# Kernel tuning notes

Measured on AMD Instinct MI355X. Metric: run time of the kernel, lower is better.

Reference implementation:

```python
import jax, jax.numpy as jnp
import numpy as np
import math

NUM_HEADS = 4
NUM_GROUPS = 16
EPS = 1e-5


def setup_inputs() -> dict:
    key = jax.random.key(0)
    ks = jax.random.split(key, 4)
    C = 256
    x = jax.random.normal(ks[0], (1, C, 16, 16, 16), dtype=jnp.float32)
    gn_gamma = jnp.ones((C,), dtype=jnp.float32)
    gn_beta = jnp.zeros((C,), dtype=jnp.float32)
    # conv3d 1x1 kernels == plain matrices [out_ch, in_ch]
    w_qkv = jax.random.normal(ks[1], (3 * C, C), dtype=jnp.float32) * (1.0 / math.sqrt(C))
    w_proj = jax.random.normal(ks[2], (C, C), dtype=jnp.float32) * (1.0 / math.sqrt(C))
    b_proj = jnp.zeros((C,), dtype=jnp.float32)
    return {"x": x, "gn_gamma": gn_gamma, "gn_beta": gn_beta,
            "w_qkv": w_qkv, "w_proj": w_proj, "b_proj": b_proj}


def reference(x, gn_gamma, gn_beta, w_qkv, w_proj, b_proj):
    B, C, H, W, D = x.shape
    N = H * W * D
    heads = NUM_HEADS
    d = C // heads

    xf = x.reshape(B, C, N)  # [B, C, N]

    # GroupNorm(16, C) with affine params
    xg = xf.reshape(B, NUM_GROUPS, C // NUM_GROUPS, N)
    mu = jnp.mean(xg, axis=(2, 3), keepdims=True)
    var = jnp.var(xg, axis=(2, 3), keepdims=True)
    xn = ((xg - mu) * jax.lax.rsqrt(var + EPS)).reshape(B, C, N)
    xn = xn * gn_gamma[None, :, None] + gn_beta[None, :, None]

    # 1x1 conv QKV: [B, 3C, N]
    qkv = jnp.einsum('oc,bcn->bon', w_qkv, xn)
    # torch: qkv.reshape(B*heads, 3d, N).chunk(3, dim=1)
    qkv = qkv.reshape(B * heads, 3 * d, N)
    q, k, v = qkv[:, :d], qkv[:, d:2 * d], qkv[:, 2 * d:]

    scale = 1.0 / math.sqrt(math.sqrt(d))
    attn = jnp.einsum('bct,bcs->bts', q * scale, k * scale)  # [B*heads, N, N]
    attn = jax.nn.softmax(attn, axis=-1)
    h = jnp.einsum('bts,bcs->bct', attn, v)  # [B*heads, d, N]

    h = h.reshape(B, C, N)
    out = jnp.einsum('oc,bcn->bon', w_proj, h) + b_proj[None, :, None]
    return (out + xf).reshape(B, C, H, W, D)
```

## Files before the change

### kernel.cpp

```cpp
#include <hip/hip_runtime.h>
#include <math.h>

#define N_TOK 4096
#define C_CH  256
#define SPLITS 4

typedef short bf16x8 __attribute__((ext_vector_type(8)));
typedef float f32x4  __attribute__((ext_vector_type(4)));
typedef unsigned short u16;

__device__ __forceinline__ u16 f2bf(float f) {
    union { float f; unsigned u; } v; v.f = f;
    unsigned r = v.u + 0x7FFF + ((v.u >> 16) & 1);
    return (u16)(r >> 16);
}
__device__ __forceinline__ float bf2f(u16 b) {
    union { unsigned u; float f; } v; v.u = ((unsigned)b) << 16;
    return v.f;
}
__device__ __forceinline__ unsigned packtr(float a, float b) {
    union { float f; unsigned u; } ua, ub; ua.f = a; ub.f = b;
    return __builtin_amdgcn_perm(ub.u, ua.u, 0x07060302u);
}

__global__ __launch_bounds__(256) void wcvt(const float* __restrict__ wqkv,
                                            const float* __restrict__ wproj,
                                            u16* __restrict__ wq, u16* __restrict__ wp) {
    int i = blockIdx.x * 256 + threadIdx.x;
    if (i < 196608) {
        int row = i >> 8;
        float s = ((row % 192) < 64) ? 0.125f : 1.0f;
        wq[i] = f2bf(wqkv[i] * s);
    } else {
        wp[i - 196608] = f2bf(wproj[i - 196608]);
    }
}

__global__ __launch_bounds__(256) void gn_part(const float* __restrict__ x,
                                               float2* __restrict__ part) {
    const int b = blockIdx.x, tid = threadIdx.x;
    const int lane = tid & 63, wave = tid >> 6;
    const float4* xp = (const float4*)x + b * 1024;
    float s = 0.f, ss = 0.f;
#pragma unroll
    for (int k = 0; k < 4; ++k) {
        float4 v = xp[tid + k * 256];
        s  += v.x + v.y + v.z + v.w;
        ss += v.x * v.x + v.y * v.y + v.z * v.z + v.w * v.w;
    }
#pragma unroll
    for (int off = 1; off < 64; off <<= 1) {
        s  += __shfl_xor(s, off, 64);
        ss += __shfl_xor(ss, off, 64);
    }
    __shared__ float rs[4], rss[4];
    if (lane == 0) { rs[wave] = s; rss[wave] = ss; }
    __syncthreads();
    if (tid == 0) part[b] = make_float2(rs[0]+rs[1]+rs[2]+rs[3], rss[0]+rss[1]+rss[2]+rss[3]);
}

__global__ void gn_fin(const float2* __restrict__ part, float* __restrict__ stats) {
    int g = threadIdx.x;
    if (g < 16) {
        float s = 0.f, ss = 0.f;
        for (int j = 0; j < 16; ++j) { float2 p = part[g * 16 + j]; s += p.x; ss += p.y; }
        float mu = s / 65536.f;
        float var = ss / 65536.f - mu * mu;
        stats[g * 2] = mu;
        stats[g * 2 + 1] = rsqrtf(var + 1e-5f);
    }
}

__global__ __launch_bounds__(256) void norm_t(const float* __restrict__ x,
                                              const float* __restrict__ stats,
                                              const float* __restrict__ gamma,
                                              const float* __restrict__ beta,
                                              u16* __restrict__ xt) {
    const int tb = blockIdx.x * 64, cb = blockIdx.y * 64;
    const int tid = threadIdx.x;
    __shared__ float T[64][65];
#pragma unroll
    for (int it = 0; it < 16; ++it) {
        int idx = tid + it * 256;
        int c = idx >> 6, t = idx & 63;
        int cg = cb + c;
        float mu = stats[(cg >> 4) * 2], rstd = stats[(cg >> 4) * 2 + 1];
        T[c][t] = (x[cg * N_TOK + tb + t] - mu) * rstd * gamma[cg] + beta[cg];
    }
    __syncthreads();
#pragma unroll
    for (int it = 0; it < 16; ++it) {
        int idx = tid + it * 256;
        int t = idx >> 6, c = idx & 63;
        xt[(tb + t) * C_CH + cb + c] = f2bf(T[c][t]);
    }
}

__global__ __launch_bounds__(256) void qkv_gemm(const u16* __restrict__ wq,
                                                const u16* __restrict__ xt,
                                                u16* __restrict__ QT,
                                                u16* __restrict__ KTm,
                                                u16* __restrict__ Vc) {
    const int nb = blockIdx.x * 64;
    const int mo = blockIdx.y * 64 + (threadIdx.x >> 6) * 16;
    const int lane = threadIdx.x & 63;
    const int quad = lane >> 4, low = lane & 15;

    f32x4 acc[4] = {f32x4{0,0,0,0}, f32x4{0,0,0,0}, f32x4{0,0,0,0}, f32x4{0,0,0,0}};
#pragma unroll
    for (int kc = 0; kc < 8; ++kc) {
        bf16x8 af = *(const bf16x8*)(wq + (mo + low) * 256 + kc * 32 + quad * 8);
#pragma unroll
        for (int nt = 0; nt < 4; ++nt) {
            bf16x8 bf_ = *(const bf16x8*)(xt + (nb + nt * 16 + low) * 256 + kc * 32 + quad * 8);
            acc[nt] = __builtin_amdgcn_mfma_f32_16x16x32_bf16(af, bf_, acc[nt], 0, 0, 0);
        }
    }
#pragma unroll
    for (int r = 0; r < 4; ++r) {
        int o = mo + quad * 4 + r;
        int head = o / 192, rem = o % 192, c = rem & 63;
#pragma unroll
        for (int nt = 0; nt < 4; ++nt) {
            int tok = nb + nt * 16 + low;
            u16 v = f2bf(acc[nt][r]);
            if (rem < 64)       QT [(head * N_TOK + tok) * 64 + c] = v;
            else if (rem < 128) KTm[(head * N_TOK + tok) * 64 + c] = v;
            else                Vc [(head * 64 + c) * N_TOK + tok] = v;
        }
    }
}

__global__ __launch_bounds__(256, 2) void attn_kernel(const u16* __restrict__ QT,
                                                      const u16* __restrict__ KTm,
                                                      const u16* __restrict__ Vc,
                                                      u16* __restrict__ Op,
                                                      float* __restrict__ Lp) {
    const int head = blockIdx.y, split = blockIdx.z;
    const int qb   = blockIdx.x * 128;
    const int tid  = threadIdx.x;
    const int wave = tid >> 6, lane = tid & 63;
    const int quad = lane >> 4, low = lane & 15;

    const u16* Qh = QT  + head * N_TOK * 64;
    const u16* Kh = KTm + head * N_TOK * 64 + split * 1024 * 64;
    const u16* Vh = Vc  + head * 64 * N_TOK + split * 1024;

    __shared__ u16 Ks[64 * 64];
    __shared__ u16 Vs[64 * 64];
    __shared__ u16 Ps[4 * 32 * 64];
    u16* Pw = Ps + wave * 2048;

    bf16x8 ones;
#pragma unroll
    for (int i = 0; i < 8; ++i) ones[i] = (short)0x3F80;

    bf16x8 bq[2][2];
#pragma unroll
    for (int tn = 0; tn < 2; ++tn)
#pragma unroll
        for (int kh = 0; kh < 2; ++kh)
            bq[tn][kh] = *(const bf16x8*)(Qh + (qb + wave * 32 + tn * 16 + low) * 64 + kh * 32 + quad * 8);

    f32x4 oa[2][4], lC[2];
#pragma unroll
    for (int mt = 0; mt < 2; ++mt) {
        lC[mt] = f32x4{0,0,0,0};
#pragma unroll
        for (int cn = 0; cn < 4; ++cn) oa[mt][cn] = f32x4{0,0,0,0};
    }

    const int sA = tid >> 3, gA = tid & 7;
    const int swA = ((gA ^ (sA & 7)) * 8);
    const int swB = ((gA ^ ((sA + 32) & 7)) * 8);
    uint4 pk0 = *(const uint4*)(Kh + sA * 64 + gA * 8);
    uint4 pk1 = *(const uint4*)(Kh + (sA + 32) * 64 + gA * 8);
    uint4 pv0 = *(const uint4*)(Vh + sA * N_TOK + gA * 8);
    uint4 pv1 = *(const uint4*)(Vh + (sA + 32) * N_TOK + gA * 8);

    const int low7 = low & 7;

    for (int kt = 0; kt < 16; ++kt) {
        __syncthreads();
        *(uint4*)(Ks + sA * 64 + swA) = pk0;
        *(uint4*)(Ks + (sA + 32) * 64 + swB) = pk1;
        *(uint4*)(Vs + sA * 64 + swA) = pv0;
        *(uint4*)(Vs + (sA + 32) * 64 + swB) = pv1;
        if (kt < 15) {
            int sb2 = (kt + 1) * 64;
            pk0 = *(const uint4*)(Kh + (sb2 + sA) * 64 + gA * 8);
            pk1 = *(const uint4*)(Kh + (sb2 + sA + 32) * 64 + gA * 8);
            pv0 = *(const uint4*)(Vh + sA * N_TOK + sb2 + gA * 8);
            pv1 = *(const uint4*)(Vh + (sA + 32) * N_TOK + sb2 + gA * 8);
        }
        __syncthreads();

        f32x4 sa[4][2];
#pragma unroll
        for (int sm = 0; sm < 4; ++sm)
#pragma unroll
            for (int tn = 0; tn < 2; ++tn) sa[sm][tn] = f32x4{0,0,0,0};
#pragma unroll
        for (int kh = 0; kh < 2; ++kh)
#pragma unroll
            for (int sm = 0; sm < 4; ++sm) {
                bf16x8 ak = *(const bf16x8*)(Ks + (sm * 16 + low) * 64 + (((quad + 4 * kh) ^ low7) * 8));
#pragma unroll
                for (int tn = 0; tn < 2; ++tn)
                    sa[sm][tn] = __builtin_amdgcn_mfma_f32_16x16x32_bf16(ak, bq[tn][kh], sa[sm][tn], 0, 0, 0);
            }

#pragma unroll
        for (int sm = 0; sm < 4; ++sm)
#pragma unroll
            for (int tn = 0; tn < 2; ++tn) {
                float p0 = __expf(sa[sm][tn][0]);
                float p1 = __expf(sa[sm][tn][1]);
                float p2 = __expf(sa[sm][tn][2]);
                float p3 = __expf(sa[sm][tn][3]);
                uint2 pk; pk.x = packtr(p0, p1); pk.y = packtr(p2, p3);
                int t = tn * 16 + low;
                int sw = ((sm * 2 + (quad >> 1)) ^ low7);
                *(uint2*)(Pw + t * 64 + sw * 8 + (quad & 1) * 4) = pk;
            }
        asm volatile("s_waitcnt lgkmcnt(0)" ::: "memory");

#pragma unroll
        for (int kh = 0; kh < 2; ++kh) {
            bf16x8 ap0 = *(const bf16x8*)(Pw + (low) * 64      + (((quad + 4 * kh) ^ low7) * 8));
            bf16x8 ap1 = *(const bf16x8*)(Pw + (16 + low) * 64 + (((quad + 4 * kh) ^ low7) * 8));
            lC[0] = __builtin_amdgcn_mfma_f32_16x16x32_bf16(ap0, ones, lC[0], 0, 0, 0);
            lC[1] = __builtin_amdgcn_mfma_f32_16x16x32_bf16(ap1, ones, lC[1], 0, 0, 0);
#pragma unroll
            for (int cn = 0; cn < 4; ++cn) {
                bf16x8 bv = *(const bf16x8*)(Vs + (cn * 16 + low) * 64 + (((quad + 4 * kh) ^ low7) * 8));
                oa[0][cn] = __builtin_amdgcn_mfma_f32_16x16x32_bf16(ap0, bv, oa[0][cn], 0, 0, 0);
                oa[1][cn] = __builtin_amdgcn_mfma_f32_16x16x32_bf16(ap1, bv, oa[1][cn], 0, 0, 0);
            }
        }
    }

    const int sh = (split * 4 + head) * N_TOK;
#pragma unroll
    for (int mt = 0; mt < 2; ++mt)
#pragma unroll
        for (int r = 0; r < 4; ++r) {
            int t = qb + wave * 32 + mt * 16 + quad * 4 + r;
            if (low == 0) Lp[sh + t] = lC[mt][r];
#pragma unroll
            for (int cn = 0; cn < 4; ++cn)
                Op[(sh + t) * 64 + cn * 16 + low] = f2bf(oa[mt][cn][r]);
        }
}

__global__ __launch_bounds__(256) void combine(const u16* __restrict__ Op,
                                               const float* __restrict__ Lp,
                                               u16* __restrict__ hT) {
    int row = blockIdx.x * 4 + (threadIdx.x >> 6);
    int head = row >> 12, t = row & 4095, c = threadIdx.x & 63;
    float o = 0.f, l = 0.f;
#pragma unroll
    for (int sp = 0; sp < SPLITS; ++sp) {
        int b = (sp * 4 + head) * N_TOK + t;
        o += bf2f(Op[b * 64 + c]);
        l += Lp[b];
    }
    hT[t * C_CH + head * 64 + c] = f2bf(o / l);
}

__global__ __launch_bounds__(256) void proj_gemm(const u16* __restrict__ wp,
                                                 const u16* __restrict__ hT,
                                                 const float* __restrict__ bias,
                                                 const float* __restrict__ xres,
                                                 float* __restrict__ out) {
    const int nb = blockIdx.x * 32;
    const int mo = blockIdx.y * 64 + (threadIdx.x >> 6) * 16;
    const int lane = threadIdx.x & 63;
    const int quad = lane >> 4, low = lane & 15;

    f32x4 acc[2] = {f32x4{0,0,0,0}, f32x4{0,0,0,0}};
#pragma unroll
    for (int kc = 0; kc < 8; ++kc) {
        bf16x8 af = *(const bf16x8*)(wp + (mo + low) * 256 + kc * 32 + quad * 8);
#pragma unroll
        for (int nt = 0; nt < 2; ++nt) {
            bf16x8 bf_ = *(const bf16x8*)(hT + (nb + nt * 16 + low) * 256 + kc * 32 + quad * 8);
            acc[nt] = __builtin_amdgcn_mfma_f32_16x16x32_bf16(af, bf_, acc[nt], 0, 0, 0);
        }
    }
#pragma unroll
    for (int r = 0; r < 4; ++r) {
        int o = mo + quad * 4 + r;
        float bv = bias[o];
#pragma unroll
        for (int nt = 0; nt < 2; ++nt) {
            int tok = nb + nt * 16 + low;
            out[o * N_TOK + tok] = acc[nt][r] + bv + xres[o * N_TOK + tok];
        }
    }
}

extern "C" void kernel_launch(void* const* d_in, const int* in_sizes, int n_in,
                              void* d_out, int out_size, void* d_ws, size_t ws_size,
                              hipStream_t stream) {
    const float* x      = (const float*)d_in[0];
    const float* gamma  = (const float*)d_in[1];
    const float* beta   = (const float*)d_in[2];
    const float* w_qkv  = (const float*)d_in[3];
    const float* w_proj = (const float*)d_in[4];
    const float* b_proj = (const float*)d_in[5];
    float* out = (float*)d_out;

    char* base = (char*)d_ws;
    u16*    Op    = (u16*)base;
    u16*    xt    = (u16*)base;
    float*  Lp    = (float*)(base + 8388608);
    float*  stats = (float*)(base + 8650752);
    float2* part  = (float2*)(base + 8654848);
    u16*    wq    = (u16*)(base + 8658944);
    u16*    wp    = (u16*)(base + 9052160);
    u16*    QT    = (u16*)(base + 9183232);
    u16*    hT    = QT;
    u16*    KTm   = (u16*)(base + 11280384);
    u16*    Vc    = (u16*)(base + 13377536);

    wcvt      <<<1024, 256, 0, stream>>>(w_qkv, w_proj, wq, wp);
    gn_part   <<<256, 256, 0, stream>>>(x, part);
    gn_fin    <<<1, 64, 0, stream>>>(part, stats);
    norm_t    <<<dim3(64, 4),  256, 0, stream>>>(x, stats, gamma, beta, xt);
    qkv_gemm  <<<dim3(64, 12), 256, 0, stream>>>(wq, xt, QT, KTm, Vc);
    attn_kernel<<<dim3(32, 4, SPLITS), 256, 0, stream>>>(QT, KTm, Vc, Op, Lp);
    combine   <<<4096, 256, 0, stream>>>(Op, Lp, hT);
    proj_gemm <<<dim3(128, 4), 256, 0, stream>>>(wp, hT, b_proj, x, out);
}
```

Measured before the change: 130.2 us.

## Fuse prep kernels, restructure attention with in-block KV split and register fragments

Merges weight conversion and GroupNorm partial sums into one launch, and folds the group-stat finalization into norm_t. The attention kernel now gives each block 64 queries, with each wave covering an interleaved quarter of the keys. K and V fragments are loaded straight from global memory into double-buffered registers instead of being staged through shared memory. The separate split-combine kernel is replaced by an in-block reduction through shared memory, and exp is swapped for exp2 with the log2e factor folded into the Q weight scale. This drops kernel launches and the Op/Lp round trip, at the cost of fewer attention blocks (256), higher register pressure at occupancy 1, and uncoalesced direct global fragment loads.

```diff
diff --git a/kernel.cpp b/kernel.cpp
--- a/kernel.cpp
+++ b/kernel.cpp
@@ -3,7 +3,6 @@
 
 #define N_TOK 4096
 #define C_CH  256
-#define SPLITS 4
 
 typedef short bf16x8 __attribute__((ext_vector_type(8)));
 typedef float f32x4  __attribute__((ext_vector_type(4)));
@@ -14,78 +13,79 @@
     unsigned r = v.u + 0x7FFF + ((v.u >> 16) & 1);
     return (u16)(r >> 16);
 }
-__device__ __forceinline__ float bf2f(u16 b) {
-    union { unsigned u; float f; } v; v.u = ((unsigned)b) << 16;
-    return v.f;
-}
 __device__ __forceinline__ unsigned packtr(float a, float b) {
     union { float f; unsigned u; } ua, ub; ua.f = a; ub.f = b;
     return __builtin_amdgcn_perm(ub.u, ua.u, 0x07060302u);
 }
 
-__global__ __launch_bounds__(256) void wcvt(const float* __restrict__ wqkv,
+__global__ __launch_bounds__(256) void prep(const float* __restrict__ wqkv,
                                             const float* __restrict__ wproj,
-                                            u16* __restrict__ wq, u16* __restrict__ wp) {
-    int i = blockIdx.x * 256 + threadIdx.x;
-    if (i < 196608) {
-        int row = i >> 8;
-        float s = ((row % 192) < 64) ? 0.125f : 1.0f;
-        wq[i] = f2bf(wqkv[i] * s);
+                                            const float* __restrict__ x,
+                                            u16* __restrict__ wq, u16* __restrict__ wp,
+                                            float2* __restrict__ part) {
+    const int b = blockIdx.x, tid = threadIdx.x;
+    __shared__ float rs[4], rss[4];
+    if (b < 1024) {
+        int i = b * 256 + tid;
+        if (i < 196608) {
+            int row = i >> 8;
+            float s = ((row % 192) < 64) ? 0.18033688f : 1.0f;
+            wq[i] = f2bf(wqkv[i] * s);
+        } else {
+            wp[i - 196608] = f2bf(wproj[i - 196608]);
+        }
     } else {
-        wp[i - 196608] = f2bf(wproj[i - 196608]);
-    }
-}
-
-__global__ __launch_bounds__(256) void gn_part(const float* __restrict__ x,
-                                               float2* __restrict__ part) {
-    const int b = blockIdx.x, tid = threadIdx.x;
-    const int lane = tid & 63, wave = tid >> 6;
-    const float4* xp = (const float4*)x + b * 1024;
-    float s = 0.f, ss = 0.f;
-#pragma unroll
-    for (int k = 0; k < 4; ++k) {
-        float4 v = xp[tid + k * 256];
-        s  += v.x + v.y + v.z + v.w;
-        ss += v.x * v.x + v.y * v.y + v.z * v.z + v.w * v.w;
-    }
-#pragma unroll
-    for (int off = 1; off < 64; off <<= 1) {
-        s  += __shfl_xor(s, off, 64);
-        ss += __shfl_xor(ss, off, 64);
-    }
-    __shared__ float rs[4], rss[4];
-    if (lane == 0) { rs[wave] = s; rss[wave] = ss; }
-    __syncthreads();
-    if (tid == 0) part[b] = make_float2(rs[0]+rs[1]+rs[2]+rs[3], rss[0]+rss[1]+rss[2]+rss[3]);
-}
-
-__global__ void gn_fin(const float2* __restrict__ part, float* __restrict__ stats) {
-    int g = threadIdx.x;
-    if (g < 16) {
+        const int bb = b - 1024;
+        const int lane = tid & 63, wave = tid >> 6;
+        const float4* xp = (const float4*)x + bb * 1024;
         float s = 0.f, ss = 0.f;
-        for (int j = 0; j < 16; ++j) { float2 p = part[g * 16 + j]; s += p.x; ss += p.y; }
-        float mu = s / 65536.f;
-        float var = ss / 65536.f - mu * mu;
-        stats[g * 2] = mu;
-        stats[g * 2 + 1] = rsqrtf(var + 1e-5f);
+#pragma unroll
+        for (int k = 0; k < 4; ++k) {
+            float4 v = xp[tid + k * 256];
+            s  += v.x + v.y + v.z + v.w;
+            ss += v.x * v.x + v.y * v.y + v.z * v.z + v.w * v.w;
+        }
+#pragma unroll
+        for (int off = 1; off < 64; off <<= 1) {
+            s  += __shfl_xor(s, off, 64);
+            ss += __shfl_xor(ss, off, 64);
+        }
+        if (lane == 0) { rs[wave] = s; rss[wave] = ss; }
+        __syncthreads();
+        if (tid == 0) part[bb] = make_float2(rs[0]+rs[1]+rs[2]+rs[3], rss[0]+rss[1]+rss[2]+rss[3]);
     }
 }
 
 __global__ __launch_bounds__(256) void norm_t(const float* __restrict__ x,
-                                              const float* __restrict__ stats,
+                                              const float2* __restrict__ part,
                                               const float* __restrict__ gamma,
                                               const float* __restrict__ beta,
                                               u16* __restrict__ xt) {
     const int tb = blockIdx.x * 64, cb = blockIdx.y * 64;
     const int tid = threadIdx.x;
+    __shared__ float sst[8];
     __shared__ float T[64][65];
+    if (tid < 64) {
+        float2 p = part[(blockIdx.y * 4 + (tid >> 4)) * 16 + (tid & 15)];
+        float s = p.x, ss = p.y;
+#pragma unroll
+        for (int off = 1; off < 16; off <<= 1) {
+            s += __shfl_xor(s, off, 64); ss += __shfl_xor(ss, off, 64);
+        }
+        if ((tid & 15) == 0) {
+            float mu = s / 65536.f;
+            float var = ss / 65536.f - mu * mu;
+            sst[(tid >> 4) * 2] = mu;
+            sst[(tid >> 4) * 2 + 1] = rsqrtf(var + 1e-5f);
+        }
+    }
+    __syncthreads();
 #pragma unroll
     for (int it = 0; it < 16; ++it) {
         int idx = tid + it * 256;
         int c = idx >> 6, t = idx & 63;
-        int cg = cb + c;
-        float mu = stats[(cg >> 4) * 2], rstd = stats[(cg >> 4) * 2 + 1];
-        T[c][t] = (x[cg * N_TOK + tb + t] - mu) * rstd * gamma[cg] + beta[cg];
+        int cg = cb + c, gl = c >> 4;
+        T[c][t] = (x[cg * N_TOK + tb + t] - sst[gl * 2]) * sst[gl * 2 + 1] * gamma[cg] + beta[cg];
     }
     __syncthreads();
 #pragma unroll
@@ -131,141 +131,150 @@
     }
 }
 
-__global__ __launch_bounds__(256, 2) void attn_kernel(const u16* __restrict__ QT,
+struct Frags { bf16x8 ak[4][2]; bf16x8 bv[2][4]; };
+
+__global__ __launch_bounds__(256, 1) void attn_kernel(const u16* __restrict__ QT,
                                                       const u16* __restrict__ KTm,
                                                       const u16* __restrict__ Vc,
-                                                      u16* __restrict__ Op,
-                                                      float* __restrict__ Lp) {
-    const int head = blockIdx.y, split = blockIdx.z;
-    const int qb   = blockIdx.x * 128;
+                                                      u16* __restrict__ hT) {
+    const int head = blockIdx.y;
+    const int qb   = blockIdx.x * 64;
     const int tid  = threadIdx.x;
     const int wave = tid >> 6, lane = tid & 63;
     const int quad = lane >> 4, low = lane & 15;
+    const int low7 = low & 7;
 
     const u16* Qh = QT  + head * N_TOK * 64;
-    const u16* Kh = KTm + head * N_TOK * 64 + split * 1024 * 64;
-    const u16* Vh = Vc  + head * 64 * N_TOK + split * 1024;
-
-    __shared__ u16 Ks[64 * 64];
-    __shared__ u16 Vs[64 * 64];
-    __shared__ u16 Ps[4 * 32 * 64];
-    u16* Pw = Ps + wave * 2048;
+    const u16* Kh = KTm + head * N_TOK * 64;
+    const u16* Vh = Vc  + head * 64 * N_TOK;
+
+    __shared__ union {
+        u16 ps[4][4096];
+        struct { float buf[2][64][65]; float lb[2][64]; } cb;
+    } sm;
+    u16* Pw = sm.ps[wave];
 
     bf16x8 ones;
 #pragma unroll
     for (int i = 0; i < 8; ++i) ones[i] = (short)0x3F80;
 
-    bf16x8 bq[2][2];
-#pragma unroll
-    for (int tn = 0; tn < 2; ++tn)
+    bf16x8 bq[4][2];
+#pragma unroll
+    for (int tn = 0; tn < 4; ++tn)
 #pragma unroll
         for (int kh = 0; kh < 2; ++kh)
-            bq[tn][kh] = *(const bf16x8*)(Qh + (qb + wave * 32 + tn * 16 + low) * 64 + kh * 32 + quad * 8);
-
-    f32x4 oa[2][4], lC[2];
-#pragma unroll
-    for (int mt = 0; mt < 2; ++mt) {
-        lC[mt] = f32x4{0,0,0,0};
-#pragma unroll
-        for (int cn = 0; cn < 4; ++cn) oa[mt][cn] = f32x4{0,0,0,0};
-    }
-
-    const int sA = tid >> 3, gA = tid & 7;
-    const int swA = ((gA ^ (sA & 7)) * 8);
-    const int swB = ((gA ^ ((sA + 32) & 7)) * 8);
-    uint4 pk0 = *(const uint4*)(Kh + sA * 64 + gA * 8);
-    uint4 pk1 = *(const uint4*)(Kh + (sA + 32) * 64 + gA * 8);
-    uint4 pv0 = *(const uint4*)(Vh + sA * N_TOK + gA * 8);
-    uint4 pv1 = *(const uint4*)(Vh + (sA + 32) * N_TOK + gA * 8);
-
-    const int low7 = low & 7;
-
-    for (int kt = 0; kt < 16; ++kt) {
-        __syncthreads();
-        *(uint4*)(Ks + sA * 64 + swA) = pk0;
-        *(uint4*)(Ks + (sA + 32) * 64 + swB) = pk1;
-        *(uint4*)(Vs + sA * 64 + swA) = pv0;
-        *(uint4*)(Vs + (sA + 32) * 64 + swB) = pv1;
-        if (kt < 15) {
-            int sb2 = (kt + 1) * 64;
-            pk0 = *(const uint4*)(Kh + (sb2 + sA) * 64 + gA * 8);
-            pk1 = *(const uint4*)(Kh + (sb2 + sA + 32) * 64 + gA * 8);
-            pv0 = *(const uint4*)(Vh + sA * N_TOK + sb2 + gA * 8);
-            pv1 = *(const uint4*)(Vh + (sA + 32) * N_TOK + sb2 + gA * 8);
-        }
-        __syncthreads();
-
-        f32x4 sa[4][2];
-#pragma unroll
-        for (int sm = 0; sm < 4; ++sm)
-#pragma unroll
-            for (int tn = 0; tn < 2; ++tn) sa[sm][tn] = f32x4{0,0,0,0};
+            bq[tn][kh] = *(const bf16x8*)(Qh + (qb + tn * 16 + low) * 64 + kh * 32 + quad * 8);
+
+    f32x4 oa[4][4], lC[4];
+#pragma unroll
+    for (int tm = 0; tm < 4; ++tm) {
+        lC[tm] = f32x4{0,0,0,0};
+#pragma unroll
+        for (int cn = 0; cn < 4; ++cn) oa[tm][cn] = f32x4{0,0,0,0};
+    }
+
+    auto load_frags = [&](Frags& F, int sbase) {
+#pragma unroll
+        for (int sq = 0; sq < 4; ++sq)
+#pragma unroll
+            for (int kh = 0; kh < 2; ++kh)
+                F.ak[sq][kh] = *(const bf16x8*)(Kh + (sbase + sq * 16 + low) * 64 + kh * 32 + quad * 8);
+#pragma unroll
+        for (int f = 0; f < 2; ++f)
+#pragma unroll
+            for (int cn = 0; cn < 4; ++cn)
+                F.bv[f][cn] = *(const bf16x8*)(Vh + (cn * 16 + low) * N_TOK + sbase + f * 32 + quad * 8);
+    };
+
+    auto compute_tile = [&](const Frags& F) {
+        f32x4 sa[4][4];
+#pragma unroll
+        for (int sq = 0; sq < 4; ++sq)
+#pragma unroll
+            for (int tn = 0; tn < 4; ++tn) sa[sq][tn] = f32x4{0,0,0,0};
 #pragma unroll
         for (int kh = 0; kh < 2; ++kh)
 #pragma unroll
-            for (int sm = 0; sm < 4; ++sm) {
-                bf16x8 ak = *(const bf16x8*)(Ks + (sm * 16 + low) * 64 + (((quad + 4 * kh) ^ low7) * 8));
-#pragma unroll
-                for (int tn = 0; tn < 2; ++tn)
-                    sa[sm][tn] = __builtin_amdgcn_mfma_f32_16x16x32_bf16(ak, bq[tn][kh], sa[sm][tn], 0, 0, 0);
-            }
-
-#pragma unroll
-        for (int sm = 0; sm < 4; ++sm)
-#pragma unroll
-            for (int tn = 0; tn < 2; ++tn) {
-                float p0 = __expf(sa[sm][tn][0]);
-                float p1 = __expf(sa[sm][tn][1]);
-                float p2 = __expf(sa[sm][tn][2]);
-                float p3 = __expf(sa[sm][tn][3]);
+            for (int sq = 0; sq < 4; ++sq)
+#pragma unroll
+                for (int tn = 0; tn < 4; ++tn)
+                    sa[sq][tn] = __builtin_amdgcn_mfma_f32_16x16x32_bf16(F.ak[sq][kh], bq[tn][kh], sa[sq][tn], 0, 0, 0);
+#pragma unroll
+        for (int sq = 0; sq < 4; ++sq)
+#pragma unroll
+            for (int tn = 0; tn < 4; ++tn) {
+                float p0 = __builtin_amdgcn_exp2f(sa[sq][tn][0]);
+                float p1 = __builtin_amdgcn_exp2f(sa[sq][tn][1]);
+                float p2 = __builtin_amdgcn_exp2f(sa[sq][tn][2]);
+                float p3 = __builtin_amdgcn_exp2f(sa[sq][tn][3]);
                 uint2 pk; pk.x = packtr(p0, p1); pk.y = packtr(p2, p3);
-                int t = tn * 16 + low;
-                int sw = ((sm * 2 + (quad >> 1)) ^ low7);
-                *(uint2*)(Pw + t * 64 + sw * 8 + (quad & 1) * 4) = pk;
+                int u = (sq * 2 + (quad >> 1)) ^ low7;
+                *(uint2*)(Pw + (tn * 16 + low) * 64 + u * 8 + (quad & 1) * 4) = pk;
             }
         asm volatile("s_waitcnt lgkmcnt(0)" ::: "memory");
-
-#pragma unroll
-        for (int kh = 0; kh < 2; ++kh) {
-            bf16x8 ap0 = *(const bf16x8*)(Pw + (low) * 64      + (((quad + 4 * kh) ^ low7) * 8));
-            bf16x8 ap1 = *(const bf16x8*)(Pw + (16 + low) * 64 + (((quad + 4 * kh) ^ low7) * 8));
-            lC[0] = __builtin_amdgcn_mfma_f32_16x16x32_bf16(ap0, ones, lC[0], 0, 0, 0);
-            lC[1] = __builtin_amdgcn_mfma_f32_16x16x32_bf16(ap1, ones, lC[1], 0, 0, 0);
-#pragma unroll
-            for (int cn = 0; cn < 4; ++cn) {
-                bf16x8 bv = *(const bf16x8*)(Vs + (cn * 16 + low) * 64 + (((quad + 4 * kh) ^ low7) * 8));
-                oa[0][cn] = __builtin_amdgcn_mfma_f32_16x16x32_bf16(ap0, bv, oa[0][cn], 0, 0, 0);
-                oa[1][cn] = __builtin_amdgcn_mfma_f32_16x16x32_bf16(ap1, bv, oa[1][cn], 0, 0, 0);
+#pragma unroll
+        for (int tm = 0; tm < 4; ++tm)
+#pragma unroll
+            for (int f = 0; f < 2; ++f) {
+                bf16x8 ap = *(const bf16x8*)(Pw + (tm * 16 + low) * 64 + (((f * 4 + quad) ^ low7) * 8));
+                lC[tm] = __builtin_amdgcn_mfma_f32_16x16x32_bf16(ap, ones, lC[tm], 0, 0, 0);
+#pragma unroll
+                for (int cn = 0; cn < 4; ++cn)
+                    oa[tm][cn] = __builtin_amdgcn_mfma_f32_16x16x32_bf16(ap, F.bv[f][cn], oa[tm][cn], 0, 0, 0);
             }
-        }
-    }
-
-    const int sh = (split * 4 + head) * N_TOK;
-#pragma unroll
-    for (int mt = 0; mt < 2; ++mt)
-#pragma unroll
-        for (int r = 0; r < 4; ++r) {
-            int t = qb + wave * 32 + mt * 16 + quad * 4 + r;
-            if (low == 0) Lp[sh + t] = lC[mt][r];
-#pragma unroll
-            for (int cn = 0; cn < 4; ++cn)
-                Op[(sh + t) * 64 + cn * 16 + low] = f2bf(oa[mt][cn][r]);
-        }
-}
-
-__global__ __launch_bounds__(256) void combine(const u16* __restrict__ Op,
-                                               const float* __restrict__ Lp,
-                                               u16* __restrict__ hT) {
-    int row = blockIdx.x * 4 + (threadIdx.x >> 6);
-    int head = row >> 12, t = row & 4095, c = threadIdx.x & 63;
-    float o = 0.f, l = 0.f;
-#pragma unroll
-    for (int sp = 0; sp < SPLITS; ++sp) {
-        int b = (sp * 4 + head) * N_TOK + t;
-        o += bf2f(Op[b * 64 + c]);
-        l += Lp[b];
-    }
-    hT[t * C_CH + head * 64 + c] = f2bf(o / l);
+    };
+
+    Frags Fa, Fb;
+    load_frags(Fa, wave * 64);
+#pragma unroll 1
+    for (int i = 0; i < 16; i += 2) {
+        load_frags(Fb, (wave + 4 * (i + 1)) * 64);
+        compute_tile(Fa);
+        if (i + 2 < 16) load_frags(Fa, (wave + 4 * (i + 2)) * 64);
+        compute_tile(Fb);
+    }
+
+    __syncthreads();
+    if ((wave & 1) == 0) {
+        int bsel = wave >> 1;
+#pragma unroll
+        for (int tm = 0; tm < 4; ++tm) {
+#pragma unroll
+            for (int r = 0; r < 4; ++r) {
+                int t = tm * 16 + quad * 4 + r;
+                if (low == 0) sm.cb.lb[bsel][t] = lC[tm][r];
+#pragma unroll
+                for (int cn = 0; cn < 4; ++cn)
+                    sm.cb.buf[bsel][t][cn * 16 + low] = oa[tm][cn][r];
+            }
+        }
+    }
+    __syncthreads();
+    if ((wave & 1) == 1) {
+        int bsel = wave >> 1;
+#pragma unroll
+        for (int tm = 0; tm < 4; ++tm) {
+#pragma unroll
+            for (int r = 0; r < 4; ++r) {
+                int t = tm * 16 + quad * 4 + r;
+                if (low == 0) sm.cb.lb[bsel][t] += lC[tm][r];
+#pragma unroll
+                for (int cn = 0; cn < 4; ++cn)
+                    sm.cb.buf[bsel][t][cn * 16 + low] += oa[tm][cn][r];
+            }
+        }
+    }
+    __syncthreads();
+    {
+        int t = tid >> 2, c0 = (tid & 3) * 16;
+        float li = 1.f / (sm.cb.lb[0][t] + sm.cb.lb[1][t]);
+#pragma unroll
+        for (int j = 0; j < 16; ++j) {
+            int c = c0 + j;
+            float o = (sm.cb.buf[0][t][c] + sm.cb.buf[1][t][c]) * li;
+            hT[(qb + t) * C_CH + head * 64 + c] = f2bf(o);
+        }
+    }
 }
 
 __global__ __launch_bounds__(256) void proj_gemm(const u16* __restrict__ wp,
@@ -312,24 +321,18 @@
     float* out = (float*)d_out;
 
     char* base = (char*)d_ws;
-    u16*    Op    = (u16*)base;
-    u16*    xt    = (u16*)base;
-    float*  Lp    = (float*)(base + 8388608);
-    float*  stats = (float*)(base + 8650752);
-    float2* part  = (float2*)(base + 8654848);
-    u16*    wq    = (u16*)(base + 8658944);
-    u16*    wp    = (u16*)(base + 9052160);
-    u16*    QT    = (u16*)(base + 9183232);
-    u16*    hT    = QT;
-    u16*    KTm   = (u16*)(base + 11280384);
-    u16*    Vc    = (u16*)(base + 13377536);
-
-    wcvt      <<<1024, 256, 0, stream>>>(w_qkv, w_proj, wq, wp);
-    gn_part   <<<256, 256, 0, stream>>>(x, part);
-    gn_fin    <<<1, 64, 0, stream>>>(part, stats);
-    norm_t    <<<dim3(64, 4),  256, 0, stream>>>(x, stats, gamma, beta, xt);
+    float2* part = (float2*)base;
+    u16*    wq   = (u16*)(base + 4096);
+    u16*    wp   = (u16*)(base + 397312);
+    u16*    xt   = (u16*)(base + 528384);
+    u16*    QT   = (u16*)(base + 2625536);
+    u16*    KTm  = (u16*)(base + 4722688);
+    u16*    Vc   = (u16*)(base + 6819840);
+    u16*    hT   = (u16*)(base + 8916992);
+
+    prep      <<<1280, 256, 0, stream>>>(w_qkv, w_proj, x, wq, wp, part);
+    norm_t    <<<dim3(64, 4),  256, 0, stream>>>(x, part, gamma, beta, xt);
     qkv_gemm  <<<dim3(64, 12), 256, 0, stream>>>(wq, xt, QT, KTm, Vc);
-    attn_kernel<<<dim3(32, 4, SPLITS), 256, 0, stream>>>(QT, KTm, Vc, Op, Lp);
-    combine   <<<4096, 256, 0, stream>>>(Op, Lp, hT);
+    attn_kernel<<<dim3(64, 4), 256, 0, stream>>>(QT, KTm, Vc, hT);
     proj_gemm <<<dim3(128, 4), 256, 0, stream>>>(wp, hT, b_proj, x, out);
 }
```

Result: slower. 132.9 us (+2.0%).
